# Kernel tuning notes

Measured on AMD Instinct MI355X. Metric: run time of the kernel, lower is better.

## Reference

```python
import jax, jax.numpy as jnp
import numpy as np

SHIFT_MIN, SHIFT_MAX = -14.0, 0.0  # deepshift range for weight_bits=5: (-(2**4-2), 0)


def shift_quant(w):
    """Quantize weights to signed powers of two (bit-shift weights), STE form."""
    sign = jnp.sign(w)
    shift = jnp.clip(jnp.round(jnp.log2(jnp.abs(w) + 1e-12)), SHIFT_MIN, SHIFT_MAX)
    q = sign * jnp.exp2(shift)
    return w + jax.lax.stop_gradient(q - w)


def moe_fc(t, wg, w0, b0, w1, b1):
    """Top-1 routing over 2 experts: expert0 dense Linear, expert1 shift-quantized Linear.
    t: [T, C]; weights torch-layout [out, in]. With top_k=1 the softmaxed top-k gate is 1.0,
    so combine is a hard select of the chosen expert's output."""
    logits = t @ wg                      # [T, 2]
    pick0 = (jnp.argmax(logits, axis=-1) == 0)[:, None]
    y0 = t @ w0.T + b0                   # dense expert
    y1 = t @ shift_quant(w1).T + b1      # shift expert
    return jnp.where(pick0, y0, y1)


def setup_inputs() -> dict:
    key = jax.random.key(0)
    ks = jax.random.split(key, 10)
    B, N, C, Dh = 16, 1024, 512, 2048
    s = 0.02
    return {
        "x": jax.random.normal(ks[0], (B, N, C), jnp.float32),
        "H": 32,
        "W": 32,
        "wg1": jax.random.normal(ks[1], (C, 2), jnp.float32) * s,
        "fc1_w0": jax.random.normal(ks[2], (Dh, C), jnp.float32) * s,
        "fc1_b0": jnp.zeros((Dh,), jnp.float32),
        "fc1_w1": jax.random.normal(ks[3], (Dh, C), jnp.float32) * s,
        "fc1_b1": jnp.zeros((Dh,), jnp.float32),
        "dw_w": jax.random.normal(ks[4], (Dh, 1, 3, 3), jnp.float32) * np.sqrt(2.0 / 9.0),
        "dw_b": jnp.zeros((Dh,), jnp.float32),
        "wg2": jax.random.normal(ks[5], (Dh, 2), jnp.float32) * s,
        "fc2_w0": jax.random.normal(ks[6], (C, Dh), jnp.float32) * s,
        "fc2_b0": jnp.zeros((C,), jnp.float32),
        "fc2_w1": jax.random.normal(ks[7], (C, Dh), jnp.float32) * s,
        "fc2_b1": jnp.zeros((C,), jnp.float32),
    }


def reference(x, H, W, wg1, fc1_w0, fc1_b0, fc1_w1, fc1_b1, dw_w, dw_b,
              wg2, fc2_w0, fc2_b0, fc2_w1, fc2_b1):
    B, N, C = x.shape
    Dh = fc1_w0.shape[0]
    # fc1 MoE
    h = moe_fc(x.reshape(-1, C), wg1, fc1_w0, fc1_b0, fc1_w1, fc1_b1)  # [B*N, Dh]
    # DWConv 3x3 depthwise, NCHW
    h = h.reshape(B, N, Dh).transpose(0, 2, 1).reshape(B, Dh, H, W)
    h = jax.lax.conv_general_dilated(
        h, dw_w, window_strides=(1, 1), padding="SAME",
        dimension_numbers=("NCHW", "OIHW", "NCHW"), feature_group_count=Dh)
    h = h + dw_b[None, :, None, None]
    h = h.reshape(B, Dh, N).transpose(0, 2, 1)  # [B, N, Dh]
    # GELU (exact, as nn.GELU default); dropout p=0 -> identity
    h = jax.nn.gelu(h, approximate=False)
    # fc2 MoE
    y = moe_fc(h.reshape(-1, Dh), wg2, fc2_w0, fc2_b0, fc2_w1, fc2_b1)
    return y.reshape(B, N, -1)
```

## Files before the change

kernel.cpp:

```cpp
#include <hip/hip_runtime.h>
#include <hip/hip_bf16.h>


#define TOKS  16384
#define CIN   512
#define DHID  2048

typedef __attribute__((ext_vector_type(8))) __bf16 bf16x8;
typedef __attribute__((ext_vector_type(4))) float  f32x4;
typedef __attribute__((ext_vector_type(4))) float  float4v;
typedef __attribute__((ext_vector_type(4))) unsigned short ushort4v;
typedef __attribute__((ext_vector_type(8))) unsigned short ushort8;

__device__ __forceinline__ unsigned short f2bf(float f) {
  union { float f; unsigned int u; } a; a.f = f;
  unsigned int u = a.u;
  unsigned int r = u + 0x7FFFu + ((u >> 16) & 1u);
  return (unsigned short)(r >> 16);
}
__device__ __forceinline__ float bf2f(unsigned short h) {
  union { unsigned int u; float f; } a; a.u = ((unsigned int)h) << 16;
  return a.f;
}

__device__ __forceinline__ float squant(float w) {
  if (w == 0.0f) return 0.0f;
  float aw = fabsf(w) + 1e-12f;
  union { float f; unsigned u; } a; a.f = aw;
  int e = (int)((a.u >> 23) & 0xFFu) - 127;
  unsigned frac = a.u & 0x7FFFFFu;
  int shift = e + (frac >= 0x3504F4u ? 1 : 0);
  shift = min(max(shift, -14), 0);
  union { unsigned u; float f; } q; q.u = (unsigned)(shift + 127) << 23;
  return (w > 0.0f) ? q.f : -q.f;
}

__device__ __forceinline__ float gelu_fast(float s) {
  float z = fabsf(s) * 0.70710678118654752f;
  float zz = z * z;
#if __has_builtin(__builtin_amdgcn_exp2f)
  float e = __builtin_amdgcn_exp2f(zz * -1.4426950408889634f);
#else
  float e = exp2f(zz * -1.4426950408889634f);
#endif
  float d = fmaf(0.3275911f, z, 1.0f);
#if __has_builtin(__builtin_amdgcn_rcpf)
  float t = __builtin_amdgcn_rcpf(d);
#else
  float t = 1.0f / d;
#endif
  float p = fmaf(1.061405429f, t, -1.453152027f);
  p = fmaf(p, t, 1.421413741f);
  p = fmaf(p, t, -0.284496736f);
  p = fmaf(p, t, 0.254829592f);
  p = p * t;
  float erfz = fmaf(-p, e, 1.0f);
  float er = (s < 0.0f) ? -erfz : erfz;
  return 0.5f * s * (1.0f + er);
}

#define GLDS16(gp, lp) __builtin_amdgcn_global_load_lds(                      \
    (const __attribute__((address_space(1))) void*)(gp),                      \
    (__attribute__((address_space(3))) void*)(lp), 16, 0, 0)

#define SBAR()  { __builtin_amdgcn_s_barrier(); __builtin_amdgcn_sched_barrier(0); }
#define VMCNT(n) asm volatile("s_waitcnt vmcnt(" #n ")" ::: "memory")

__global__ void k_prep(const float* __restrict__ w0, const float* __restrict__ w1,
                       const float* __restrict__ w20, const float* __restrict__ w21,
                       unsigned short* __restrict__ w0hi, unsigned short* __restrict__ w0lo,
                       unsigned short* __restrict__ w1q, unsigned short* __restrict__ w20b,
                       unsigned short* __restrict__ w21b,
                       const float* __restrict__ x, const float* __restrict__ wg1,
                       unsigned short* __restrict__ xhi, unsigned short* __restrict__ xlo,
                       unsigned char* __restrict__ pick1) {
  __shared__ float wg[1024];
  const int t = threadIdx.x;
  if (blockIdx.x < 4096) {
    int i = blockIdx.x * 256 + t;
    float v = w0[i];
    unsigned short h = f2bf(v);
    w0hi[i] = h;
    w0lo[i] = f2bf(v - bf2f(h));
    w1q[i]  = f2bf(squant(w1[i]));
    w20b[i] = f2bf(w20[i]);
    w21b[i] = f2bf(squant(w21[i]));
    return;
  }
  const int bid = blockIdx.x - 4096;
  #pragma unroll
  for (int i = 0; i < 4; ++i) wg[t + i * 256] = wg1[t + i * 256];
  __syncthreads();
  const int tok = bid * 4 + (t >> 6);
  const int l = t & 63;
  const float* xr = x + (size_t)tok * CIN + l * 8;
  float4v v0 = *(const float4v*)xr;
  float4v v1 = *(const float4v*)(xr + 4);
  float s0 = 0.f, s1 = 0.f;
  ushort8 hv, lv;
  #pragma unroll
  for (int j = 0; j < 8; ++j) {
    float v = (j < 4) ? v0[j] : v1[j - 4];
    unsigned short h = f2bf(v);
    hv[j] = h;
    lv[j] = f2bf(v - bf2f(h));
    int c = l * 8 + j;
    s0 += v * wg[c * 2];
    s1 += v * wg[c * 2 + 1];
  }
  *(ushort8*)&xhi[(size_t)tok * CIN + l * 8] = hv;
  *(ushort8*)&xlo[(size_t)tok * CIN + l * 8] = lv;
  for (int m = 32; m; m >>= 1) { s0 += __shfl_xor(s0, m); s1 += __shfl_xor(s1, m); }
  if (l == 0) pick1[tok] = (s0 >= s1) ? 0 : 1;
}

__global__ void k_scan(const unsigned char* __restrict__ pick, int* __restrict__ perm,
                       int* __restrict__ n0buf) {
  __shared__ int wpre[17];
  const int t = threadIdx.x;
  const int lane = t & 63, w = t >> 6;
  unsigned char loc[16]; int c0 = 0;
  #pragma unroll
  for (int i = 0; i < 16; ++i) { loc[i] = pick[t * 16 + i]; c0 += (loc[i] == 0); }
  int s = c0;
  #pragma unroll
  for (int off = 1; off < 64; off <<= 1) {
    int v = __shfl_up(s, off);
    if (lane >= off) s += v;
  }
  if (lane == 63) wpre[w + 1] = s;
  if (t == 0) wpre[0] = 0;
  __syncthreads();
  if (t == 0) {
    for (int j = 1; j <= 16; ++j) wpre[j] += wpre[j - 1];
    n0buf[0] = wpre[16];
  }
  __syncthreads();
  int total0 = wpre[16];
  int pre0 = wpre[w] + s - c0;
  int pre1 = t * 16 - pre0;
  int p0 = pre0, p1 = total0 + pre1;
  #pragma unroll
  for (int i = 0; i < 16; ++i) {
    int tok = t * 16 + i;
    if (loc[i] == 0) perm[p0++] = tok; else perm[p1++] = tok;
  }
}

__launch_bounds__(256, 2)
__global__ void k_fc1(const unsigned short* __restrict__ xhi,
                      const unsigned short* __restrict__ xlo,
                      const unsigned short* __restrict__ w0hi,
                      const unsigned short* __restrict__ w0lo,
                      const unsigned short* __restrict__ w1q,
                      const float* __restrict__ b0, const float* __restrict__ b1,
                      const int* __restrict__ perm, const int* __restrict__ n0buf,
                      float* __restrict__ h32) {
  __shared__ unsigned short sm[24576];
  const int n0 = n0buf[0];
  const int t = threadIdx.x, wv = t >> 6, ln = t & 63;
  const int lr = ln & 15, lg = ln >> 4;
  const int g = blockIdx.x, q = g >> 3;
  const int tok0 = ((g & 7) + ((q >> 4) << 3)) * 128;
  const int nbase = (q & 15) * 128;
  const int wm = (wv >> 1) * 64, wn = (wv & 1) * 64;
  const bool hasE0 = (tok0 < n0), hasE1 = (tok0 + 128 > n0);

  int rowoff[4];
  #pragma unroll
  for (int mt = 0; mt < 4; ++mt)
    rowoff[mt] = perm[tok0 + wm + (mt << 4) + lr] * CIN + (lg << 3);

  const int swsrc = (((ln & 3) ^ ((ln >> 3) & 3)) << 3);
  const int swrd  = ((lg ^ ((lr >> 1) & 3)) << 3);

  f32x4 acc[4][4];

  auto ZERO = [&]() {
    #pragma unroll
    for (int i = 0; i < 4; ++i)
      #pragma unroll
      for (int j = 0; j < 4; ++j) acc[i][j] = f32x4{0.f, 0.f, 0.f, 0.f};
  };
  auto LOADA = [&](bf16x8 (&ah)[4], bf16x8 (&al)[4], int kt) {
    const int k0 = kt * 32;
    #pragma unroll
    for (int mt = 0; mt < 4; ++mt) {
      ah[mt] = *(const bf16x8*)&xhi[rowoff[mt] + k0];
      al[mt] = *(const bf16x8*)&xlo[rowoff[mt] + k0];
    }
  };

  auto RUN_E0 = [&]() {
    auto STAGEB = [&](int kt, int db) {
      const int k0 = kt * 32;
      #pragma unroll
      for (int s = 0; s < 2; ++s) {
        const int rowblk = s * 4 + wv;
        size_t gb = (size_t)(nbase + (rowblk << 4) + (ln >> 2)) * CIN + k0 + swsrc;
        GLDS16(w0hi + gb, &sm[db * 8192 + (rowblk << 9)]);
        GLDS16(w0lo + gb, &sm[db * 8192 + 4096 + (rowblk << 9)]);
      }
    };
    auto COMPUTE = [&](const bf16x8 (&ah)[4], const bf16x8 (&al)[4], int db) {
      __builtin_amdgcn_s_setprio(1);
      #pragma unroll
      for (int nt = 0; nt < 4; ++nt) {
        int bb = db * 8192 + (wn + (nt << 4) + lr) * 32 + swrd;
        bf16x8 bh = *(const bf16x8*)&sm[bb];
        bf16x8 bl = *(const bf16x8*)&sm[bb + 4096];
        #pragma unroll
        for (int mt = 0; mt < 4; ++mt) {
          acc[mt][nt] = __builtin_amdgcn_mfma_f32_16x16x32_bf16(ah[mt], bh, acc[mt][nt], 0, 0, 0);
          acc[mt][nt] = __builtin_amdgcn_mfma_f32_16x16x32_bf16(al[mt], bh, acc[mt][nt], 0, 0, 0);
          acc[mt][nt] = __builtin_amdgcn_mfma_f32_16x16x32_bf16(ah[mt], bl, acc[mt][nt], 0, 0, 0);
        }
      }
      __builtin_amdgcn_s_setprio(0);
    };
    bf16x8 Ah0[4], Al0[4], Ah1[4], Al1[4];
    LOADA(Ah0, Al0, 0);
    STAGEB(0, 0);
    STAGEB(1, 1);
    for (int kt = 0; kt < 14; kt += 2) {
      SBAR();
      LOADA(Ah1, Al1, kt + 1);
      STAGEB(kt + 2, (kt + 2) % 3);
      VMCNT(16);
      SBAR();
      COMPUTE(Ah0, Al0, kt % 3);
      SBAR();
      LOADA(Ah0, Al0, kt + 2);
      STAGEB(kt + 3, (kt + 3) % 3);
      VMCNT(16);
      SBAR();
      COMPUTE(Ah1, Al1, (kt + 1) % 3);
    }
    SBAR();
    LOADA(Ah1, Al1, 15);
    VMCNT(12);
    SBAR();
    COMPUTE(Ah0, Al0, 2);
    SBAR();
    VMCNT(0);
    SBAR();
    COMPUTE(Ah1, Al1, 0);
  };

  auto RUN_E1 = [&]() {
    auto STAGEB = [&](int kt, int db) {
      const int k0 = kt * 32;
      #pragma unroll
      for (int s = 0; s < 2; ++s) {
        const int rowblk = s * 4 + wv;
        size_t gb = (size_t)(nbase + (rowblk << 4) + (ln >> 2)) * CIN + k0 + swsrc;
        GLDS16(w1q + gb, &sm[db * 4096 + (rowblk << 9)]);
      }
    };
    auto COMPUTE = [&](const bf16x8 (&ah)[4], const bf16x8 (&al)[4], int db) {
      __builtin_amdgcn_s_setprio(1);
      #pragma unroll
      for (int nt = 0; nt < 4; ++nt) {
        bf16x8 bq = *(const bf16x8*)&sm[db * 4096 + (wn + (nt << 4) + lr) * 32 + swrd];
        #pragma unroll
        for (int mt = 0; mt < 4; ++mt) {
          acc[mt][nt] = __builtin_amdgcn_mfma_f32_16x16x32_bf16(ah[mt], bq, acc[mt][nt], 0, 0, 0);
          acc[mt][nt] = __builtin_amdgcn_mfma_f32_16x16x32_bf16(al[mt], bq, acc[mt][nt], 0, 0, 0);
        }
      }
      __builtin_amdgcn_s_setprio(0);
    };
    bf16x8 Ah0[4], Al0[4], Ah1[4], Al1[4];
    LOADA(Ah0, Al0, 0);
    STAGEB(0, 0);
    STAGEB(1, 1);
    for (int kt = 0; kt < 14; kt += 2) {
      SBAR();
      LOADA(Ah1, Al1, kt + 1);
      STAGEB(kt + 2, (kt + 2) % 3);
      VMCNT(12);
      SBAR();
      COMPUTE(Ah0, Al0, kt % 3);
      SBAR();
      LOADA(Ah0, Al0, kt + 2);
      STAGEB(kt + 3, (kt + 3) % 3);
      VMCNT(12);
      SBAR();
      COMPUTE(Ah1, Al1, (kt + 1) % 3);
    }
    SBAR();
    LOADA(Ah1, Al1, 15);
    VMCNT(10);
    SBAR();
    COMPUTE(Ah0, Al0, 2);
    SBAR();
    VMCNT(0);
    SBAR();
    COMPUTE(Ah1, Al1, 0);
  };

  auto EPI = [&](const float* bias_v, bool isE0) {
    __syncthreads();
    float* smf = (float*)sm;
    float bi[4];
    #pragma unroll
    for (int nt = 0; nt < 4; ++nt) bi[nt] = bias_v[nbase + wn + (nt << 4) + lr];
    #pragma unroll
    for (int mt = 0; mt < 4; ++mt) {
      #pragma unroll
      for (int nt = 0; nt < 4; ++nt) {
        f32x4 v = acc[mt][nt];
        #pragma unroll
        for (int rr = 0; rr < 4; ++rr)
          smf[wv * 1088 + ((lg << 2) + rr) * 68 + (nt << 4) + lr] = v[rr] + bi[nt];
      }
      #pragma unroll
      for (int p = 0; p < 4; ++p) {
        int row = (p << 2) + (ln >> 4);
        int pos = tok0 + wm + (mt << 4) + row;
        bool sel = isE0 ? (pos < n0) : (pos >= n0);
        if (sel) {
          f32x4 vv = *(const f32x4*)&smf[wv * 1088 + row * 68 + ((ln & 15) << 2)];
          *(f32x4*)&h32[(size_t)perm[pos] * DHID + nbase + wn + ((ln & 15) << 2)] = vv;
        }
      }
    }
  };

  if (hasE0) { ZERO(); RUN_E0(); EPI(b0, true); }
  if (hasE1) {
    __syncthreads();
    ZERO(); RUN_E1(); EPI(b1, false);
  }
}

__launch_bounds__(256)
__global__ void k_conv(const float* __restrict__ h32, const float* __restrict__ dww,
                       const float* __restrict__ dwb, const float* __restrict__ wg2,
                       unsigned short* __restrict__ hb, float* __restrict__ part) {
  __shared__ float4v tile[10][32][8];
  const int dc = blockIdx.x;
  const int ys = blockIdx.y;
  const int b  = blockIdx.z;
  const int t = threadIdx.x;
  const int d0 = dc * 32, y0 = ys * 8;
  const int dl4 = t & 7, xq = t >> 3;

  #pragma unroll
  for (int ry = 0; ry < 10; ++ry) {
    int y = y0 - 1 + ry;
    float4v v = {0.f, 0.f, 0.f, 0.f};
    if (y >= 0 && y < 32)
      v = *(const float4v*)&h32[(size_t)(b * 1024 + y * 32 + xq) * DHID + d0 + dl4 * 4];
    tile[ry][xq][dl4] = v;
  }
  __syncthreads();

  const int d = d0 + dl4 * 4;
  float4v kk[9];
  #pragma unroll
  for (int i = 0; i < 9; ++i) {
    kk[i][0] = dww[(d + 0) * 9 + i]; kk[i][1] = dww[(d + 1) * 9 + i];
    kk[i][2] = dww[(d + 2) * 9 + i]; kk[i][3] = dww[(d + 3) * 9 + i];
  }
  const float4v bias = *(const float4v*)&dwb[d];
  float4v g0v, g1v;
  #pragma unroll
  for (int j = 0; j < 4; ++j) { g0v[j] = wg2[(d + j) * 2]; g1v[j] = wg2[(d + j) * 2 + 1]; }

  #pragma unroll
  for (int yy = 0; yy < 8; ++yy) {
    float4v s = bias;
    #pragma unroll
    for (int dy = 0; dy < 3; ++dy)
      #pragma unroll
      for (int dx = 0; dx < 3; ++dx) {
        int xs = xq + dx - 1;
        if (xs >= 0 && xs < 32) {
          float4v v = tile[yy + dy][xs][dl4];
          float4v k = kk[dy * 3 + dx];
          s[0] += v[0] * k[0]; s[1] += v[1] * k[1];
          s[2] += v[2] * k[2]; s[3] += v[3] * k[3];
        }
      }
    float4v gg;
    #pragma unroll
    for (int j = 0; j < 4; ++j) gg[j] = gelu_fast(s[j]);
    int tok = b * 1024 + (y0 + yy) * 32 + xq;
    ushort4v hv;
    #pragma unroll
    for (int j = 0; j < 4; ++j) hv[j] = f2bf(gg[j]);
    *(ushort4v*)&hb[(size_t)tok * DHID + d] = hv;
    float p0 = gg[0] * g0v[0] + gg[1] * g0v[1] + gg[2] * g0v[2] + gg[3] * g0v[3];
    float p1 = gg[0] * g1v[0] + gg[1] * g1v[1] + gg[2] * g1v[2] + gg[3] * g1v[3];
    p0 += __shfl_xor(p0, 1); p0 += __shfl_xor(p0, 2); p0 += __shfl_xor(p0, 4);
    p1 += __shfl_xor(p1, 1); p1 += __shfl_xor(p1, 2); p1 += __shfl_xor(p1, 4);
    if (dl4 == 0) {
      part[(size_t)dc * TOKS + tok] = p0;
      part[(size_t)(64 + dc) * TOKS + tok] = p1;
    }
  }
}

__global__ void k_gate2(const float* __restrict__ part, unsigned char* __restrict__ pick2) {
  int tok = blockIdx.x * 256 + threadIdx.x;
  float s0 = 0.f, s1 = 0.f;
  for (int i = 0; i < 64; ++i) {
    s0 += part[(size_t)i * TOKS + tok];
    s1 += part[(size_t)(64 + i) * TOKS + tok];
  }
  pick2[tok] = (s0 >= s1) ? 0 : 1;
}

__launch_bounds__(256, 2)
__global__ void k_fc2(const unsigned short* __restrict__ hb,
                      const unsigned short* __restrict__ w20b,
                      const unsigned short* __restrict__ w21b,
                      const float* __restrict__ b20, const float* __restrict__ b21,
                      const int* __restrict__ perm, const int* __restrict__ n0buf,
                      float* __restrict__ out) {
  __shared__ unsigned short sm[24576];
  const int n0 = n0buf[0];
  const int t = threadIdx.x, wv = t >> 6, ln = t & 63;
  const int lr = ln & 15, lg = ln >> 4;
  const int g = blockIdx.x, q = g >> 3;
  const int tok0 = ((g & 7) + ((q >> 2) << 3)) * 128;
  const int nbase = (q & 3) * 128;
  const int wm = (wv >> 1) * 64, wn = (wv & 1) * 64;
  const bool hasE0 = (tok0 < n0), hasE1 = (tok0 + 128 > n0);

  int rowoff[4];
  #pragma unroll
  for (int mt = 0; mt < 4; ++mt)
    rowoff[mt] = perm[tok0 + wm + (mt << 4) + lr] * DHID + (lg << 3);

  const int swsrc = (((ln & 3) ^ ((ln >> 3) & 3)) << 3);
  const int swrd  = ((lg ^ ((lr >> 1) & 3)) << 3);

  f32x4 acc[4][4];
  auto ZERO = [&]() {
    #pragma unroll
    for (int i = 0; i < 4; ++i)
      #pragma unroll
      for (int j = 0; j < 4; ++j) acc[i][j] = f32x4{0.f, 0.f, 0.f, 0.f};
  };
  auto LOADA = [&](bf16x8 (&a)[8], int kt) {
    #pragma unroll
    for (int ks = 0; ks < 2; ++ks) {
      const int k0 = kt * 64 + ks * 32;
      #pragma unroll
      for (int mt = 0; mt < 4; ++mt)
        a[ks * 4 + mt] = *(const bf16x8*)&hb[rowoff[mt] + k0];
    }
  };

  auto RUN = [&](const unsigned short* __restrict__ wb) {
    auto STAGEB = [&](int kt, int db) {
      #pragma unroll
      for (int ks = 0; ks < 2; ++ks) {
        const int k0 = kt * 64 + ks * 32;
        #pragma unroll
        for (int s = 0; s < 2; ++s) {
          const int rowblk = s * 4 + wv;
          size_t gb = (size_t)(nbase + (rowblk << 4) + (ln >> 2)) * DHID + k0 + swsrc;
          GLDS16(wb + gb, &sm[db * 8192 + ks * 4096 + (rowblk << 9)]);
        }
      }
    };
    auto COMPUTE = [&](const bf16x8 (&a)[8], int db) {
      __builtin_amdgcn_s_setprio(1);
      #pragma unroll
      for (int ks = 0; ks < 2; ++ks) {
        #pragma unroll
        for (int nt = 0; nt < 4; ++nt) {
          bf16x8 bf = *(const bf16x8*)&sm[db * 8192 + ks * 4096 + (wn + (nt << 4) + lr) * 32 + swrd];
          #pragma unroll
          for (int mt = 0; mt < 4; ++mt)
            acc[mt][nt] = __builtin_amdgcn_mfma_f32_16x16x32_bf16(a[ks * 4 + mt], bf, acc[mt][nt], 0, 0, 0);
        }
      }
      __builtin_amdgcn_s_setprio(0);
    };
    bf16x8 A0[8], A1[8];
    LOADA(A0, 0);
    STAGEB(0, 0);
    STAGEB(1, 1);
    for (int kt = 0; kt < 30; kt += 2) {
      SBAR();
      LOADA(A1, kt + 1);
      STAGEB(kt + 2, (kt + 2) % 3);
      VMCNT(16);
      SBAR();
      COMPUTE(A0, kt % 3);
      SBAR();
      LOADA(A0, kt + 2);
      STAGEB(kt + 3, (kt + 3) % 3);
      VMCNT(16);
      SBAR();
      COMPUTE(A1, (kt + 1) % 3);
    }
    SBAR();
    LOADA(A1, 31);
    VMCNT(12);
    SBAR();
    COMPUTE(A0, 0);
    SBAR();
    VMCNT(0);
    SBAR();
    COMPUTE(A1, 1);
  };

  auto EPI = [&](const float* bias_v, bool isE0) {
    __syncthreads();
    float* smf = (float*)sm;
    float bi[4];
    #pragma unroll
    for (int nt = 0; nt < 4; ++nt) bi[nt] = bias_v[nbase + wn + (nt << 4) + lr];
    #pragma unroll
    for (int mt = 0; mt < 4; ++mt) {
      #pragma unroll
      for (int nt = 0; nt < 4; ++nt) {
        f32x4 v = acc[mt][nt];
        #pragma unroll
        for (int rr = 0; rr < 4; ++rr)
          smf[wv * 1088 + ((lg << 2) + rr) * 68 + (nt << 4) + lr] = v[rr] + bi[nt];
      }
      #pragma unroll
      for (int p = 0; p < 4; ++p) {
        int row = (p << 2) + (ln >> 4);
        int pos = tok0 + wm + (mt << 4) + row;
        bool sel = isE0 ? (pos < n0) : (pos >= n0);
        if (sel) {
          f32x4 vv = *(const f32x4*)&smf[wv * 1088 + row * 68 + ((ln & 15) << 2)];
          *(f32x4*)&out[(size_t)perm[pos] * CIN + nbase + wn + ((ln & 15) << 2)] = vv;
        }
      }
    }
  };

  if (hasE0) { ZERO(); RUN(w20b); EPI(b20, true); }
  if (hasE1) {
    __syncthreads();
    ZERO(); RUN(w21b); EPI(b21, false);
  }
}

extern "C" void kernel_launch(void* const* d_in, const int* in_sizes, int n_in,
                              void* d_out, int out_size, void* d_ws, size_t ws_size,
                              hipStream_t stream) {
  (void)in_sizes; (void)n_in; (void)out_size; (void)ws_size;
  const float* x   = (const float*)d_in[0];
  const float* wg1 = (const float*)d_in[3];
  const float* w0  = (const float*)d_in[4];
  const float* b0  = (const float*)d_in[5];
  const float* w1  = (const float*)d_in[6];
  const float* b1  = (const float*)d_in[7];
  const float* dww = (const float*)d_in[8];
  const float* dwb = (const float*)d_in[9];
  const float* wg2 = (const float*)d_in[10];
  const float* w20 = (const float*)d_in[11];
  const float* b20 = (const float*)d_in[12];
  const float* w21 = (const float*)d_in[13];
  const float* b21 = (const float*)d_in[14];
  float* out = (float*)d_out;

  char* ws = (char*)d_ws;
  const size_t MB2 = 1u << 21;
  unsigned short* w0hi = (unsigned short*)(ws + 0 * MB2);
  unsigned short* w0lo = (unsigned short*)(ws + 1 * MB2);
  unsigned short* w1q  = (unsigned short*)(ws + 2 * MB2);
  unsigned short* w20b = (unsigned short*)(ws + 3 * MB2);
  unsigned short* w21b = (unsigned short*)(ws + 4 * MB2);
  char* p = ws + 5 * MB2;
  unsigned short* xhi = (unsigned short*)p;            p += (size_t)TOKS * CIN * 2;
  unsigned short* xlo = (unsigned short*)p;            p += (size_t)TOKS * CIN * 2;
  unsigned char* pick1 = (unsigned char*)p;            p += 65536;
  unsigned char* pick2 = (unsigned char*)p;            p += 65536;
  int* perm1 = (int*)p;                                p += TOKS * 4;
  int* perm2 = (int*)p;                                p += TOKS * 4;
  int* n0a   = (int*)p;                                p += 256;
  int* n0b   = (int*)p;                                p += 256;
  float* part = (float*)p;                             p += (size_t)TOKS * 128 * 4;
  float* h32  = (float*)p;                             p += (size_t)TOKS * DHID * 4;
  unsigned short* hb = (unsigned short*)p;

  k_prep <<<8192, 256, 0, stream>>>(w0, w1, w20, w21, w0hi, w0lo, w1q, w20b, w21b,
                                    x, wg1, xhi, xlo, pick1);
  k_scan <<<1, 1024, 0, stream>>>(pick1, perm1, n0a);
  k_fc1  <<<2048, 256, 0, stream>>>(xhi, xlo, w0hi, w0lo, w1q, b0, b1, perm1, n0a, h32);
  k_conv <<<dim3(64, 4, 16), 256, 0, stream>>>(h32, dww, dwb, wg2, hb, part);
  k_gate2<<<64, 256, 0, stream>>>(part, pick2);
  k_scan <<<1, 1024, 0, stream>>>(pick2, perm2, n0b);
  k_fc2  <<<512, 256, 0, stream>>>(hb, w20b, w21b, b20, b21, perm2, n0b, out);
}
```

Baseline: 378.7 us.

## Widen fc1/fc2 GEMM tiles to 128x256 with 8-wave blocks and double buffering

Both MoE GEMM kernels move from 256-thread blocks computing 128x128 tiles to 512-thread blocks computing 128x256 tiles, so each A fragment loaded per token block is reused across twice as many output columns. The LDS B pipeline drops from triple to double buffering to fit the larger B slab, with the vmcnt waits adjusted to match. The grouped block-index swizzle is replaced by a plain token-major mapping. In exchange, the 512-thread x2 launch bound tightens the per-wave register budget, which risks spills. fc2 now launches only 256 blocks, and the shallower prefetch may expose more memory latency.

```diff
diff --git a/kernel.cpp b/kernel.cpp
--- a/kernel.cpp
+++ b/kernel.cpp
@@ -147,7 +147,7 @@
   }
 }
 
-__launch_bounds__(256, 2)
+__launch_bounds__(512, 2)
 __global__ void k_fc1(const unsigned short* __restrict__ xhi,
                       const unsigned short* __restrict__ xlo,
                       const unsigned short* __restrict__ w0hi,
@@ -156,14 +156,14 @@
                       const float* __restrict__ b0, const float* __restrict__ b1,
                       const int* __restrict__ perm, const int* __restrict__ n0buf,
                       float* __restrict__ h32) {
-  __shared__ unsigned short sm[24576];
+  __shared__ unsigned short sm[32768];
   const int n0 = n0buf[0];
   const int t = threadIdx.x, wv = t >> 6, ln = t & 63;
   const int lr = ln & 15, lg = ln >> 4;
-  const int g = blockIdx.x, q = g >> 3;
-  const int tok0 = ((g & 7) + ((q >> 4) << 3)) * 128;
-  const int nbase = (q & 15) * 128;
-  const int wm = (wv >> 1) * 64, wn = (wv & 1) * 64;
+  const int g = blockIdx.x;
+  const int tok0 = (g & 127) * 128;
+  const int nbase = (g >> 7) * 256;
+  const int wm = (wv >> 2) * 64, wn = (wv & 3) * 64;
   const bool hasE0 = (tok0 < n0), hasE1 = (tok0 + 128 > n0);
 
   int rowoff[4];
@@ -175,7 +175,6 @@
   const int swrd  = ((lg ^ ((lr >> 1) & 3)) << 3);
 
   f32x4 acc[4][4];
-
   auto ZERO = [&]() {
     #pragma unroll
     for (int i = 0; i < 4; ++i)
@@ -196,19 +195,19 @@
       const int k0 = kt * 32;
       #pragma unroll
       for (int s = 0; s < 2; ++s) {
-        const int rowblk = s * 4 + wv;
+        const int rowblk = wv * 2 + s;
         size_t gb = (size_t)(nbase + (rowblk << 4) + (ln >> 2)) * CIN + k0 + swsrc;
-        GLDS16(w0hi + gb, &sm[db * 8192 + (rowblk << 9)]);
-        GLDS16(w0lo + gb, &sm[db * 8192 + 4096 + (rowblk << 9)]);
+        GLDS16(w0hi + gb, &sm[db * 16384 + (rowblk << 9)]);
+        GLDS16(w0lo + gb, &sm[db * 16384 + 8192 + (rowblk << 9)]);
       }
     };
     auto COMPUTE = [&](const bf16x8 (&ah)[4], const bf16x8 (&al)[4], int db) {
       __builtin_amdgcn_s_setprio(1);
       #pragma unroll
       for (int nt = 0; nt < 4; ++nt) {
-        int bb = db * 8192 + (wn + (nt << 4) + lr) * 32 + swrd;
+        int bb = db * 16384 + (wn + (nt << 4) + lr) * 32 + swrd;
         bf16x8 bh = *(const bf16x8*)&sm[bb];
-        bf16x8 bl = *(const bf16x8*)&sm[bb + 4096];
+        bf16x8 bl = *(const bf16x8*)&sm[bb + 8192];
         #pragma unroll
         for (int mt = 0; mt < 4; ++mt) {
           acc[mt][nt] = __builtin_amdgcn_mfma_f32_16x16x32_bf16(ah[mt], bh, acc[mt][nt], 0, 0, 0);
@@ -221,30 +220,30 @@
     bf16x8 Ah0[4], Al0[4], Ah1[4], Al1[4];
     LOADA(Ah0, Al0, 0);
     STAGEB(0, 0);
-    STAGEB(1, 1);
     for (int kt = 0; kt < 14; kt += 2) {
       SBAR();
       LOADA(Ah1, Al1, kt + 1);
-      STAGEB(kt + 2, (kt + 2) % 3);
-      VMCNT(16);
-      SBAR();
-      COMPUTE(Ah0, Al0, kt % 3);
+      STAGEB(kt + 1, 1);
+      VMCNT(12);
+      SBAR();
+      COMPUTE(Ah0, Al0, 0);
       SBAR();
       LOADA(Ah0, Al0, kt + 2);
-      STAGEB(kt + 3, (kt + 3) % 3);
-      VMCNT(16);
-      SBAR();
-      COMPUTE(Ah1, Al1, (kt + 1) % 3);
+      STAGEB(kt + 2, 0);
+      VMCNT(12);
+      SBAR();
+      COMPUTE(Ah1, Al1, 1);
     }
     SBAR();
     LOADA(Ah1, Al1, 15);
+    STAGEB(15, 1);
     VMCNT(12);
     SBAR();
-    COMPUTE(Ah0, Al0, 2);
+    COMPUTE(Ah0, Al0, 0);
     SBAR();
     VMCNT(0);
     SBAR();
-    COMPUTE(Ah1, Al1, 0);
+    COMPUTE(Ah1, Al1, 1);
   };
 
   auto RUN_E1 = [&]() {
@@ -252,16 +251,16 @@
       const int k0 = kt * 32;
       #pragma unroll
       for (int s = 0; s < 2; ++s) {
-        const int rowblk = s * 4 + wv;
+        const int rowblk = wv * 2 + s;
         size_t gb = (size_t)(nbase + (rowblk << 4) + (ln >> 2)) * CIN + k0 + swsrc;
-        GLDS16(w1q + gb, &sm[db * 4096 + (rowblk << 9)]);
+        GLDS16(w1q + gb, &sm[db * 8192 + (rowblk << 9)]);
       }
     };
     auto COMPUTE = [&](const bf16x8 (&ah)[4], const bf16x8 (&al)[4], int db) {
       __builtin_amdgcn_s_setprio(1);
       #pragma unroll
       for (int nt = 0; nt < 4; ++nt) {
-        bf16x8 bq = *(const bf16x8*)&sm[db * 4096 + (wn + (nt << 4) + lr) * 32 + swrd];
+        bf16x8 bq = *(const bf16x8*)&sm[db * 8192 + (wn + (nt << 4) + lr) * 32 + swrd];
         #pragma unroll
         for (int mt = 0; mt < 4; ++mt) {
           acc[mt][nt] = __builtin_amdgcn_mfma_f32_16x16x32_bf16(ah[mt], bq, acc[mt][nt], 0, 0, 0);
@@ -273,30 +272,30 @@
     bf16x8 Ah0[4], Al0[4], Ah1[4], Al1[4];
     LOADA(Ah0, Al0, 0);
     STAGEB(0, 0);
-    STAGEB(1, 1);
     for (int kt = 0; kt < 14; kt += 2) {
       SBAR();
       LOADA(Ah1, Al1, kt + 1);
-      STAGEB(kt + 2, (kt + 2) % 3);
-      VMCNT(12);
-      SBAR();
-      COMPUTE(Ah0, Al0, kt % 3);
+      STAGEB(kt + 1, 1);
+      VMCNT(10);
+      SBAR();
+      COMPUTE(Ah0, Al0, 0);
       SBAR();
       LOADA(Ah0, Al0, kt + 2);
-      STAGEB(kt + 3, (kt + 3) % 3);
-      VMCNT(12);
-      SBAR();
-      COMPUTE(Ah1, Al1, (kt + 1) % 3);
+      STAGEB(kt + 2, 0);
+      VMCNT(10);
+      SBAR();
+      COMPUTE(Ah1, Al1, 1);
     }
     SBAR();
     LOADA(Ah1, Al1, 15);
+    STAGEB(15, 1);
     VMCNT(10);
     SBAR();
-    COMPUTE(Ah0, Al0, 2);
+    COMPUTE(Ah0, Al0, 0);
     SBAR();
     VMCNT(0);
     SBAR();
-    COMPUTE(Ah1, Al1, 0);
+    COMPUTE(Ah1, Al1, 1);
   };
 
   auto EPI = [&](const float* bias_v, bool isE0) {
@@ -412,21 +411,21 @@
   pick2[tok] = (s0 >= s1) ? 0 : 1;
 }
 
-__launch_bounds__(256, 2)
+__launch_bounds__(512, 2)
 __global__ void k_fc2(const unsigned short* __restrict__ hb,
                       const unsigned short* __restrict__ w20b,
                       const unsigned short* __restrict__ w21b,
                       const float* __restrict__ b20, const float* __restrict__ b21,
                       const int* __restrict__ perm, const int* __restrict__ n0buf,
                       float* __restrict__ out) {
-  __shared__ unsigned short sm[24576];
+  __shared__ unsigned short sm[32768];
   const int n0 = n0buf[0];
   const int t = threadIdx.x, wv = t >> 6, ln = t & 63;
   const int lr = ln & 15, lg = ln >> 4;
-  const int g = blockIdx.x, q = g >> 3;
-  const int tok0 = ((g & 7) + ((q >> 2) << 3)) * 128;
-  const int nbase = (q & 3) * 128;
-  const int wm = (wv >> 1) * 64, wn = (wv & 1) * 64;
+  const int g = blockIdx.x;
+  const int tok0 = (g & 127) * 128;
+  const int nbase = (g >> 7) * 256;
+  const int wm = (wv >> 2) * 64, wn = (wv & 3) * 64;
   const bool hasE0 = (tok0 < n0), hasE1 = (tok0 + 128 > n0);
 
   int rowoff[4];
@@ -461,9 +460,9 @@
         const int k0 = kt * 64 + ks * 32;
         #pragma unroll
         for (int s = 0; s < 2; ++s) {
-          const int rowblk = s * 4 + wv;
+          const int rowblk = wv * 2 + s;
           size_t gb = (size_t)(nbase + (rowblk << 4) + (ln >> 2)) * DHID + k0 + swsrc;
-          GLDS16(wb + gb, &sm[db * 8192 + ks * 4096 + (rowblk << 9)]);
+          GLDS16(wb + gb, &sm[db * 16384 + ks * 8192 + (rowblk << 9)]);
         }
       }
     };
@@ -473,7 +472,7 @@
       for (int ks = 0; ks < 2; ++ks) {
         #pragma unroll
         for (int nt = 0; nt < 4; ++nt) {
-          bf16x8 bf = *(const bf16x8*)&sm[db * 8192 + ks * 4096 + (wn + (nt << 4) + lr) * 32 + swrd];
+          bf16x8 bf = *(const bf16x8*)&sm[db * 16384 + ks * 8192 + (wn + (nt << 4) + lr) * 32 + swrd];
           #pragma unroll
           for (int mt = 0; mt < 4; ++mt)
             acc[mt][nt] = __builtin_amdgcn_mfma_f32_16x16x32_bf16(a[ks * 4 + mt], bf, acc[mt][nt], 0, 0, 0);
@@ -484,23 +483,23 @@
     bf16x8 A0[8], A1[8];
     LOADA(A0, 0);
     STAGEB(0, 0);
-    STAGEB(1, 1);
     for (int kt = 0; kt < 30; kt += 2) {
       SBAR();
       LOADA(A1, kt + 1);
-      STAGEB(kt + 2, (kt + 2) % 3);
-      VMCNT(16);
-      SBAR();
-      COMPUTE(A0, kt % 3);
+      STAGEB(kt + 1, 1);
+      VMCNT(12);
+      SBAR();
+      COMPUTE(A0, 0);
       SBAR();
       LOADA(A0, kt + 2);
-      STAGEB(kt + 3, (kt + 3) % 3);
-      VMCNT(16);
-      SBAR();
-      COMPUTE(A1, (kt + 1) % 3);
+      STAGEB(kt + 2, 0);
+      VMCNT(12);
+      SBAR();
+      COMPUTE(A1, 1);
     }
     SBAR();
     LOADA(A1, 31);
+    STAGEB(31, 1);
     VMCNT(12);
     SBAR();
     COMPUTE(A0, 0);
@@ -587,9 +586,9 @@
   k_prep <<<8192, 256, 0, stream>>>(w0, w1, w20, w21, w0hi, w0lo, w1q, w20b, w21b,
                                     x, wg1, xhi, xlo, pick1);
   k_scan <<<1, 1024, 0, stream>>>(pick1, perm1, n0a);
-  k_fc1  <<<2048, 256, 0, stream>>>(xhi, xlo, w0hi, w0lo, w1q, b0, b1, perm1, n0a, h32);
+  k_fc1  <<<1024, 512, 0, stream>>>(xhi, xlo, w0hi, w0lo, w1q, b0, b1, perm1, n0a, h32);
   k_conv <<<dim3(64, 4, 16), 256, 0, stream>>>(h32, dww, dwb, wg2, hb, part);
   k_gate2<<<64, 256, 0, stream>>>(part, pick2);
   k_scan <<<1, 1024, 0, stream>>>(pick2, perm2, n0b);
-  k_fc2  <<<512, 256, 0, stream>>>(hb, w20b, w21b, b20, b21, perm2, n0b, out);
-}
+  k_fc2  <<<256, 512, 0, stream>>>(hb, w20b, w21b, b20, b21, perm2, n0b, out);
+}
```

New measurement: 492.7 us. 1.3x slower.
